# Optimization experiments

Hardware: AMD Instinct MI355X
Metric: run time of the kernel (lower is better)

Reference implementation:

```python
import jax, jax.numpy as jnp
import numpy as np

S = 4096      # total packed tokens
DIM = 1280    # hidden dim
H = 16        # num heads
HD = DIM // H # head dim = 80


def setup_inputs() -> dict:
    key = jax.random.key(0)
    ks = jax.random.split(key, 5)
    hidden_states = jax.random.normal(ks[0], (S, DIM), jnp.float32)
    # realistic rotary tables: [S, HD] with duplicated half-frequencies
    inv_freq = 1.0 / (10000.0 ** (np.arange(0, HD // 2, dtype=np.float64) / (HD // 2)))
    ang = np.arange(S, dtype=np.float64)[:, None] * inv_freq[None, :]          # [S, HD/2]
    emb = np.concatenate([ang, ang], axis=-1)                                   # [S, HD]
    cos = jnp.asarray(np.cos(emb), jnp.float32)
    sin = jnp.asarray(np.sin(emb), jnp.float32)
    scale = 1.0 / np.sqrt(DIM)
    qkv_w = jax.random.normal(ks[1], (3 * DIM, DIM), jnp.float32) * scale
    qkv_b = jax.random.normal(ks[2], (3 * DIM,), jnp.float32) * 0.02
    proj_w = jax.random.normal(ks[3], (DIM, DIM), jnp.float32) * scale
    proj_b = jax.random.normal(ks[4], (DIM,), jnp.float32) * 0.02
    # ragged segment boundaries: must start at 0 and end at S
    cu_seqlens = jnp.asarray([0, 300, 900, 1500, 2300, 2900, 3500, 4000, 4096], jnp.int32)
    return {
        "hidden_states": hidden_states,
        "cos": cos,
        "sin": sin,
        "qkv_w": qkv_w,
        "qkv_b": qkv_b,
        "proj_w": proj_w,
        "proj_b": proj_b,
        "cu_seqlens": cu_seqlens,
    }


def _rotate_half(x):
    x1, x2 = jnp.split(x, 2, axis=-1)
    return jnp.concatenate([-x2, x1], axis=-1)


def reference(hidden_states, cos, sin, qkv_w, qkv_b, proj_w, proj_b, cu_seqlens):
    seq_len, dim = hidden_states.shape
    hd = dim // H
    qkv = (hidden_states @ qkv_w.T + qkv_b).reshape(seq_len, 3, H, hd)
    q, k, v = qkv[:, 0], qkv[:, 1], qkv[:, 2]                 # each [S, H, hd]
    # RoPE in float32, broadcast cos/sin over heads
    c = cos[:, None, :].astype(jnp.float32)
    s = sin[:, None, :].astype(jnp.float32)
    qf = q.astype(jnp.float32)
    kf = k.astype(jnp.float32)
    q = (qf * c + _rotate_half(qf) * s).astype(q.dtype)
    k = (kf * c + _rotate_half(kf) * s).astype(k.dtype)
    # block-diagonal additive mask: segment id per token
    pos = jnp.arange(seq_len)
    seg = jnp.searchsorted(cu_seqlens[1:], pos, side='right')  # [S]
    neg = jnp.finfo(jnp.float32).min
    bias = jnp.where(seg[:, None] == seg[None, :], 0.0, neg)   # [S, S]
    attn = jnp.einsum('shd,thd->hst', q, k) / np.sqrt(hd) + bias[None]
    w = jax.nn.softmax(attn.astype(jnp.float32), axis=-1).astype(q.dtype)
    out = jnp.einsum('hst,thd->shd', w, v).reshape(seq_len, dim)
    return out @ proj_w.T + proj_b
```

## Files before the change

kernel.cpp:

```cpp
#include <hip/hip_runtime.h>
#include <hip/hip_bf16.h>
#include <stdint.h>

#define SQ 4096
#define DM 1280
#define NH 16
#define HDIM 80
#define N_QKV 3840

typedef __attribute__((ext_vector_type(8))) short short8;
typedef __attribute__((ext_vector_type(4))) float f32x4;

__device__ __forceinline__ unsigned short f2bf(float f) {
  union { float f; unsigned int u; } v; v.f = f;
  unsigned int r = v.u + 0x7FFFu + ((v.u >> 16) & 1u);
  return (unsigned short)(r >> 16);
}
__device__ __forceinline__ float bf2f(unsigned short u) {
  union { unsigned int u; float f; } v; v.u = ((unsigned int)u) << 16;
  return v.f;
}

__global__ __launch_bounds__(256) void cvt_all(const float* __restrict__ hidden,
                                               const float* __restrict__ qkv_w,
                                               const float* __restrict__ proj_w,
                                               unsigned short* __restrict__ oh,
                                               unsigned short* __restrict__ oq,
                                               unsigned short* __restrict__ op) {
  int b = blockIdx.x;
  const float* in;
  unsigned short* out;
  int base;
  if (b < 5120) { in = hidden; out = oh; base = b; }
  else if (b < 9920) { in = qkv_w; out = oq; base = b - 5120; }
  else { in = proj_w; out = op; base = b - 9920; }
  int i = base * 256 + threadIdx.x;
  float4 v = reinterpret_cast<const float4*>(in)[i];
  ushort4 o;
  o.x = f2bf(v.x); o.y = f2bf(v.y); o.z = f2bf(v.z); o.w = f2bf(v.w);
  reinterpret_cast<ushort4*>(out)[i] = o;
}

__device__ __forceinline__ void gload_lds16(const void* g, void* l) {
  __builtin_amdgcn_global_load_lds(
      (const __attribute__((address_space(1))) void*)g,
      (__attribute__((address_space(3))) void*)l, 16, 0, 0);
}

template <int OUT_BF16>
__global__ __launch_bounds__(256, 3) void gemm_bt(const unsigned short* __restrict__ A,
                                                  const unsigned short* __restrict__ B,
                                                  const float* __restrict__ bias,
                                                  void* __restrict__ C, int M, int N, int K,
                                                  int nbx) {
  __shared__ __align__(16) unsigned short As[3][128 * 32];
  __shared__ __align__(16) unsigned short Bs[3][128 * 32];
  const int tid = threadIdx.x;
  const int wave = tid >> 6, lane = tid & 63;
  const int r15 = lane & 15, kg = lane >> 4;
  const int wr = wave >> 1, wc = wave & 1;

  const int b = blockIdx.x;
  const int c = b & 7, i = b >> 3;
  const int by = (c & 3) * 8 + (i & 7);
  const int bx = (c >> 2) * (nbx >> 1) + (i >> 3);
  const int tm = by * 128, tn = bx * 128;

  f32x4 acc[4][4];
#pragma unroll
  for (int x = 0; x < 4; ++x)
#pragma unroll
    for (int j = 0; j < 4; ++j) acc[x][j] = {0.f, 0.f, 0.f, 0.f};

  const int slot0 = wave * 64 + lane;
  const int row0 = slot0 >> 2, k80 = (slot0 & 3) << 3;
  const int slot1 = slot0 + 256;
  const int row1 = slot1 >> 2, k81 = (slot1 & 3) << 3;
  const unsigned short* Arow0 = A + (size_t)(tm + row0) * K + k80;
  const unsigned short* Arow1 = A + (size_t)(tm + row1) * K + k81;
  const unsigned short* Brow0 = B + (size_t)(tn + row0) * K + k80;
  const unsigned short* Brow1 = B + (size_t)(tn + row1) * K + k81;
  const int ldsoff0 = (wave * 64) * 8;
  const int ldsoff1 = (wave * 64 + 256) * 8;

  auto stage = [&](int kt, int buf) {
    gload_lds16(Arow0 + kt, &As[buf][ldsoff0]);
    gload_lds16(Arow1 + kt, &As[buf][ldsoff1]);
    gload_lds16(Brow0 + kt, &Bs[buf][ldsoff0]);
    gload_lds16(Brow1 + kt, &Bs[buf][ldsoff1]);
  };

  const int nk = K >> 5;
  stage(0, 0);
  if (nk > 1) stage(32, 1);

  int buf = 0;
  for (int t = 0; t < nk; ++t) {
    if (t + 2 < nk) {
      stage((t + 2) << 5, (buf + 2) % 3);
      asm volatile("s_waitcnt vmcnt(8)" ::: "memory");
    } else if (t + 1 < nk) {
      asm volatile("s_waitcnt vmcnt(4)" ::: "memory");
    } else {
      asm volatile("s_waitcnt vmcnt(0)" ::: "memory");
    }
    __builtin_amdgcn_sched_barrier(0);
    __builtin_amdgcn_s_barrier();

    short8 af[4], bfr[4];
#pragma unroll
    for (int mi = 0; mi < 4; ++mi)
      af[mi] = *reinterpret_cast<const short8*>(&As[buf][(wr * 64 + mi * 16 + r15) * 32 + kg * 8]);
#pragma unroll
    for (int ni = 0; ni < 4; ++ni)
      bfr[ni] = *reinterpret_cast<const short8*>(&Bs[buf][(wc * 64 + ni * 16 + r15) * 32 + kg * 8]);
    __builtin_amdgcn_s_setprio(1);
#pragma unroll
    for (int mi = 0; mi < 4; ++mi)
#pragma unroll
      for (int ni = 0; ni < 4; ++ni)
        acc[mi][ni] = __builtin_amdgcn_mfma_f32_16x16x32_bf16(af[mi], bfr[ni], acc[mi][ni], 0, 0, 0);
    __builtin_amdgcn_s_setprio(0);

    __builtin_amdgcn_s_barrier();
    __builtin_amdgcn_sched_barrier(0);
    buf = (buf + 1) % 3;
  }

#pragma unroll
  for (int mi = 0; mi < 4; ++mi) {
#pragma unroll
    for (int ni = 0; ni < 4; ++ni) {
      int col = tn + wc * 64 + ni * 16 + r15;
      float bv = bias[col];
#pragma unroll
      for (int r = 0; r < 4; ++r) {
        int row = tm + wr * 64 + mi * 16 + kg * 4 + r;
        float v = acc[mi][ni][r] + bv;
        if (OUT_BF16)
          ((unsigned short*)C)[(size_t)row * N + col] = f2bf(v);
        else
          ((float*)C)[(size_t)row * N + col] = v;
      }
    }
  }
}

__global__ __launch_bounds__(256) void rope_v_kernel(unsigned short* __restrict__ qkv,
                                                     const float* __restrict__ cosb,
                                                     const float* __restrict__ sinb,
                                                     unsigned short* __restrict__ Vt) {
  int h = blockIdx.y, s0 = blockIdx.x * 64;
  __shared__ unsigned short vt[64][80];
  for (int e = threadIdx.x; e < 64 * 40; e += 256) {
    int sl = e / 40, dp = e % 40;
    int s = s0 + sl;
    float c = cosb[s * HDIM + dp];
    float sn = sinb[s * HDIM + dp];
    size_t qb = (size_t)s * N_QKV + h * HDIM;
    float q1 = bf2f(qkv[qb + dp]), q2 = bf2f(qkv[qb + dp + 40]);
    qkv[qb + dp] = f2bf(q1 * c - q2 * sn);
    qkv[qb + dp + 40] = f2bf(q2 * c + q1 * sn);
    size_t kb = qb + DM;
    float k1 = bf2f(qkv[kb + dp]), k2 = bf2f(qkv[kb + dp + 40]);
    qkv[kb + dp] = f2bf(k1 * c - k2 * sn);
    qkv[kb + dp + 40] = f2bf(k2 * c + k1 * sn);
    size_t vb = qb + 2 * DM;
    vt[sl][dp] = qkv[vb + dp];
    vt[sl][dp + 40] = qkv[vb + dp + 40];
  }
  __syncthreads();
  for (int e = threadIdx.x; e < HDIM * 64; e += 256) {
    int d = e >> 6, sl = e & 63;
    Vt[((size_t)h * HDIM + d) * SQ + s0 + sl] = vt[sl][d];
  }
}

template <int CTRL>
__device__ __forceinline__ float dpp_f(float x) {
  int xi = __builtin_bit_cast(int, x);
  int r = __builtin_amdgcn_update_dpp(xi, xi, CTRL, 0xf, 0xf, true);
  return __builtin_bit_cast(float, r);
}
__device__ __forceinline__ float rowmax16(float x) {
  x = fmaxf(x, dpp_f<0xB1>(x));
  x = fmaxf(x, dpp_f<0x4E>(x));
  x = fmaxf(x, dpp_f<0x141>(x));
  x = fmaxf(x, dpp_f<0x140>(x));
  return x;
}
__device__ __forceinline__ float rowsum16(float x) {
  x += dpp_f<0xB1>(x);
  x += dpp_f<0x4E>(x);
  x += dpp_f<0x141>(x);
  x += dpp_f<0x140>(x);
  return x;
}

__global__ __launch_bounds__(256, 2) void attn_kernel(const unsigned short* __restrict__ qkv,
                                                      const unsigned short* __restrict__ Vt,
                                                      const int* __restrict__ cu, int nseg,
                                                      unsigned short* __restrict__ attn_out) {
  constexpr int PROW = 68;
  __shared__ __align__(16) unsigned char Kl[2][64 * 256];
  __shared__ __align__(16) unsigned char Vl[2][80 * 128];
  __shared__ __align__(16) unsigned short Pl[4][16 * PROW];
  __shared__ int cus[32];

  const int tid = threadIdx.x;
  const int wave = tid >> 6, lane = tid & 63;
  const int r15 = lane & 15, kg = lane >> 4;
  const int s7 = r15 & 7;
  const short8 z8 = {0, 0, 0, 0, 0, 0, 0, 0};

  const int b = blockIdx.x;
  const int xcd = b & 7, j = b >> 3;
  const int h = xcd * 2 + (j >> 6);
  const int qt = j & 63;

  if (tid <= nseg) cus[tid] = cu[tid];
  __syncthreads();

  auto seg_of = [&](int pos) {
    int s2 = 0;
    for (int i2 = 1; i2 < nseg; ++i2)
      if (pos >= cus[i2]) s2 = i2;
    return s2;
  };

  const int tbase = qt * 64;
  const int wbase = tbase + wave * 16;
  int rs[4], re[4];
#pragma unroll
  for (int r = 0; r < 4; ++r) {
    int sg = seg_of(wbase + kg * 4 + r);
    rs[r] = cus[sg];
    re[r] = cus[sg + 1];
  }
  const int kb0 = cus[seg_of(tbase)] & ~63;
  const int kend = cus[seg_of(tbase + 63) + 1];
  const int nt = (kend - kb0 + 63) >> 6;

  const unsigned short* qp = qkv + (size_t)(wbase + r15) * N_QKV + h * HDIM;
  short8 qf[3];
#pragma unroll
  for (int ds = 0; ds < 3; ++ds) {
    int d0 = ds * 32 + kg * 8;
    qf[ds] = (d0 < HDIM) ? *reinterpret_cast<const short8*>(qp + d0) : z8;
  }

  float m[4] = {-1e30f, -1e30f, -1e30f, -1e30f};
  float l[4] = {0.f, 0.f, 0.f, 0.f};
  f32x4 acc[5];
#pragma unroll
  for (int dg = 0; dg < 5; ++dg) acc[dg] = {0.f, 0.f, 0.f, 0.f};

  const float scale = 0.1118033988749895f;
  const unsigned short* kbase = qkv + DM + (size_t)h * HDIM;
  const unsigned short* vbase = Vt + (size_t)h * HDIM * SQ;
  unsigned short* pw = &Pl[wave][0];
  const int wub = tid & ~63;

  auto issue_stage = [&](int kb, int buf) {
    unsigned char* kd = &Kl[buf][0];
    unsigned char* vd = &Vl[buf][0];
#pragma unroll
    for (int p = 0; p < 4; ++p) {
      int L = p * 256 + tid;
      int row = L >> 4;
      int c = (L & 15) ^ (row & 7);
      int csrc = (c < 10) ? c : 0;
      gload_lds16(kbase + (size_t)(kb + row) * N_QKV + csrc * 8,
                  kd + (p * 256 + wub) * 16);
    }
#pragma unroll
    for (int p = 0; p < 2; ++p) {
      int L = p * 256 + tid;
      int row = L >> 3;
      int c = (L & 7) ^ (row & 7);
      gload_lds16(vbase + (size_t)row * SQ + kb + c * 8,
                  vd + (p * 256 + wub) * 16);
    }
    {
      int L = 512 + (wub >> 1) + (lane & 31);
      int row = L >> 3;
      int c = (L & 7) ^ (row & 7);
      if (lane < 32)
        gload_lds16(vbase + (size_t)row * SQ + kb + c * 8,
                    vd + (512 + (wub >> 1)) * 16);
    }
  };

  issue_stage(kb0, 0);
  int cur = 0;

  for (int t = 0; t < nt; ++t) {
    const int k0 = kb0 + (t << 6);
    if (t + 1 < nt) {
      issue_stage(k0 + 64, cur ^ 1);
      asm volatile("s_waitcnt vmcnt(7)" ::: "memory");
    } else {
      asm volatile("s_waitcnt vmcnt(0)" ::: "memory");
    }
    __builtin_amdgcn_sched_barrier(0);
    __builtin_amdgcn_s_barrier();

    const unsigned char* Kc = &Kl[cur][0];
    const unsigned char* Vc = &Vl[cur][0];

    f32x4 sa[4];
#pragma unroll
    for (int g = 0; g < 4; ++g) sa[g] = {0.f, 0.f, 0.f, 0.f};
#pragma unroll
    for (int g = 0; g < 4; ++g) {
      const unsigned char* kr = Kc + ((g * 16 + r15) << 8);
#pragma unroll
      for (int ds = 0; ds < 3; ++ds) {
        int d0 = ds * 32 + kg * 8;
        short8 kf = (d0 < HDIM)
            ? *reinterpret_cast<const short8*>(kr + (((ds * 4 + kg) ^ s7) << 4))
            : z8;
        sa[g] = __builtin_amdgcn_mfma_f32_16x16x32_bf16(qf[ds], kf, sa[g], 0, 0, 0);
      }
    }

    short8 vf[5][2];
#pragma unroll
    for (int dg = 0; dg < 5; ++dg)
#pragma unroll
      for (int g2 = 0; g2 < 2; ++g2)
        vf[dg][g2] = *reinterpret_cast<const short8*>(
            Vc + ((dg * 16 + r15) << 7) + (((g2 * 4 + kg) ^ s7) << 4));

    float p[4][4], corr[4];
#pragma unroll
    for (int r = 0; r < 4; ++r) {
      float vv[4];
#pragma unroll
      for (int g = 0; g < 4; ++g) {
        int key = k0 + g * 16 + r15;
        vv[g] = (key >= rs[r] && key < re[r]) ? sa[g][r] * scale : -1e30f;
      }
      float mx = fmaxf(fmaxf(vv[0], vv[1]), fmaxf(vv[2], vv[3]));
      mx = rowmax16(mx);
      float mn = fmaxf(m[r], mx);
      float c = __expf(m[r] - mn);
      float sm = 0.f;
#pragma unroll
      for (int g = 0; g < 4; ++g) {
        p[r][g] = __expf(vv[g] - mn);
        sm += p[r][g];
      }
      sm = rowsum16(sm);
      l[r] = l[r] * c + sm;
      m[r] = mn;
      corr[r] = c;
    }
#pragma unroll
    for (int dg = 0; dg < 5; ++dg) {
      f32x4 t2 = acc[dg];
      t2[0] *= corr[0]; t2[1] *= corr[1]; t2[2] *= corr[2]; t2[3] *= corr[3];
      acc[dg] = t2;
    }

#pragma unroll
    for (int r = 0; r < 4; ++r) {
      unsigned short* prow = pw + (kg * 4 + r) * PROW;
#pragma unroll
      for (int g = 0; g < 4; ++g) prow[g * 16 + r15] = f2bf(p[r][g]);
    }
    asm volatile("s_waitcnt lgkmcnt(0)" ::: "memory");
    __builtin_amdgcn_sched_barrier(0);
    const unsigned short* prd = pw + r15 * PROW;
    union { short8 v; uint2 d[2]; } pu[2];
#pragma unroll
    for (int g2 = 0; g2 < 2; ++g2) {
      pu[g2].d[0] = *reinterpret_cast<const uint2*>(prd + g2 * 32 + kg * 8);
      pu[g2].d[1] = *reinterpret_cast<const uint2*>(prd + g2 * 32 + kg * 8 + 4);
    }

    __builtin_amdgcn_s_setprio(1);
#pragma unroll
    for (int dg = 0; dg < 5; ++dg)
#pragma unroll
      for (int g2 = 0; g2 < 2; ++g2)
        acc[dg] = __builtin_amdgcn_mfma_f32_16x16x32_bf16(pu[g2].v, vf[dg][g2], acc[dg], 0, 0, 0);
    __builtin_amdgcn_s_setprio(0);

    __builtin_amdgcn_s_barrier();
    cur ^= 1;
  }

#pragma unroll
  for (int r = 0; r < 4; ++r) {
    int row = wbase + kg * 4 + r;
    float inv = 1.0f / l[r];
#pragma unroll
    for (int dg = 0; dg < 5; ++dg)
      attn_out[(size_t)row * DM + h * HDIM + dg * 16 + r15] = f2bf(acc[dg][r] * inv);
  }
}

extern "C" void kernel_launch(void* const* d_in, const int* in_sizes, int n_in,
                              void* d_out, int out_size, void* d_ws, size_t ws_size,
                              hipStream_t stream) {
  const float* hidden = (const float*)d_in[0];
  const float* cosb = (const float*)d_in[1];
  const float* sinb = (const float*)d_in[2];
  const float* qkv_w = (const float*)d_in[3];
  const float* qkv_b = (const float*)d_in[4];
  const float* proj_w = (const float*)d_in[5];
  const float* proj_b = (const float*)d_in[6];
  const int* cu = (const int*)d_in[7];
  int nseg = in_sizes[7] - 1;
  float* out = (float*)d_out;

  char* ws = (char*)d_ws;
  unsigned short* Ah = (unsigned short*)(ws);
  unsigned short* Wq = (unsigned short*)(ws + 10485760);
  unsigned short* Wp = (unsigned short*)(ws + 10485760 + 9830400);
  unsigned short* qkvB = (unsigned short*)(ws + 23592960);
  unsigned short* Vt = (unsigned short*)(ws + 23592960 + 31457280);
  unsigned short* attn_out = Ah;

  cvt_all<<<dim3(11520), dim3(256), 0, stream>>>(hidden, qkv_w, proj_w, Ah, Wq, Wp);
  gemm_bt<1><<<dim3(960), dim3(256), 0, stream>>>(Ah, Wq, qkv_b, qkvB, SQ, N_QKV, DM, 30);
  rope_v_kernel<<<dim3(64, NH), dim3(256), 0, stream>>>(qkvB, cosb, sinb, Vt);
  attn_kernel<<<dim3(1024), dim3(256), 0, stream>>>(qkvB, Vt, cu, nseg, attn_out);
  gemm_bt<0><<<dim3(320), dim3(256), 0, stream>>>(attn_out, Wp, proj_b, out, SQ, DM, DM, 10);
}
```

Baseline: 193.7 us.

## Restructure attention loop: skip inactive tiles, defer rescale, load V directly to registers

Folds the softmax scale into Q during RoPE, removes the V shared-memory staging so V fragments are read from global memory straight into registers, and raises the occupancy target to 3 blocks per CU. Each wave now skips key tiles that fall outside its own segment range. Tiles fully inside a segment drop the masking, and when the new row max stays within a threshold of the running max, the accumulator rescale is skipped (lazy rescaling). The P buffer gets an XOR swizzle so it can be read with 16-byte loads. The risks are global-load latency for V, a shallower prefetch pipeline since the K stage is issued later and waited on with vmcnt(0), and register pressure under the tighter launch bound.

After: 306.1 us. +58.0%, slower.

```diff
diff --git a/kernel.cpp b/kernel.cpp
--- a/kernel.cpp
+++ b/kernel.cpp
@@ -150,6 +150,7 @@
                                                      const float* __restrict__ cosb,
                                                      const float* __restrict__ sinb,
                                                      unsigned short* __restrict__ Vt) {
+  const float SC = 0.1118033988749895f;
   int h = blockIdx.y, s0 = blockIdx.x * 64;
   __shared__ unsigned short vt[64][80];
   for (int e = threadIdx.x; e < 64 * 40; e += 256) {
@@ -159,8 +160,8 @@
     float sn = sinb[s * HDIM + dp];
     size_t qb = (size_t)s * N_QKV + h * HDIM;
     float q1 = bf2f(qkv[qb + dp]), q2 = bf2f(qkv[qb + dp + 40]);
-    qkv[qb + dp] = f2bf(q1 * c - q2 * sn);
-    qkv[qb + dp + 40] = f2bf(q2 * c + q1 * sn);
+    qkv[qb + dp] = f2bf((q1 * c - q2 * sn) * SC);
+    qkv[qb + dp + 40] = f2bf((q2 * c + q1 * sn) * SC);
     size_t kb = qb + DM;
     float k1 = bf2f(qkv[kb + dp]), k2 = bf2f(qkv[kb + dp + 40]);
     qkv[kb + dp] = f2bf(k1 * c - k2 * sn);
@@ -197,14 +198,12 @@
   return x;
 }
 
-__global__ __launch_bounds__(256, 2) void attn_kernel(const unsigned short* __restrict__ qkv,
+__global__ __launch_bounds__(256, 3) void attn_kernel(const unsigned short* __restrict__ qkv,
                                                       const unsigned short* __restrict__ Vt,
                                                       const int* __restrict__ cu, int nseg,
                                                       unsigned short* __restrict__ attn_out) {
-  constexpr int PROW = 68;
   __shared__ __align__(16) unsigned char Kl[2][64 * 256];
-  __shared__ __align__(16) unsigned char Vl[2][80 * 128];
-  __shared__ __align__(16) unsigned short Pl[4][16 * PROW];
+  __shared__ __align__(16) unsigned short Pl[4][16 * 64];
   __shared__ int cus[32];
 
   const int tid = threadIdx.x;
@@ -237,6 +236,10 @@
     rs[r] = cus[sg];
     re[r] = cus[sg + 1];
   }
+  const int seg_lo = seg_of(wbase), seg_hi = seg_of(wbase + 15);
+  const int w_lo = cus[seg_lo], w_hi = cus[seg_hi + 1];
+  const int rs_hi = cus[seg_hi], re_lo = cus[seg_lo + 1];
+
   const int kb0 = cus[seg_of(tbase)] & ~63;
   const int kend = cus[seg_of(tbase + 63) + 1];
   const int nt = (kend - kb0 + 63) >> 6;
@@ -255,7 +258,6 @@
 #pragma unroll
   for (int dg = 0; dg < 5; ++dg) acc[dg] = {0.f, 0.f, 0.f, 0.f};
 
-  const float scale = 0.1118033988749895f;
   const unsigned short* kbase = qkv + DM + (size_t)h * HDIM;
   const unsigned short* vbase = Vt + (size_t)h * HDIM * SQ;
   unsigned short* pw = &Pl[wave][0];
@@ -263,7 +265,6 @@
 
   auto issue_stage = [&](int kb, int buf) {
     unsigned char* kd = &Kl[buf][0];
-    unsigned char* vd = &Vl[buf][0];
 #pragma unroll
     for (int p = 0; p < 4; ++p) {
       int L = p * 256 + tid;
@@ -273,22 +274,6 @@
       gload_lds16(kbase + (size_t)(kb + row) * N_QKV + csrc * 8,
                   kd + (p * 256 + wub) * 16);
     }
-#pragma unroll
-    for (int p = 0; p < 2; ++p) {
-      int L = p * 256 + tid;
-      int row = L >> 3;
-      int c = (L & 7) ^ (row & 7);
-      gload_lds16(vbase + (size_t)row * SQ + kb + c * 8,
-                  vd + (p * 256 + wub) * 16);
-    }
-    {
-      int L = 512 + (wub >> 1) + (lane & 31);
-      int row = L >> 3;
-      int c = (L & 7) ^ (row & 7);
-      if (lane < 32)
-        gload_lds16(vbase + (size_t)row * SQ + kb + c * 8,
-                    vd + (512 + (wub >> 1)) * 16);
-    }
   };
 
   issue_stage(kb0, 0);
@@ -296,96 +281,130 @@
 
   for (int t = 0; t < nt; ++t) {
     const int k0 = kb0 + (t << 6);
-    if (t + 1 < nt) {
-      issue_stage(k0 + 64, cur ^ 1);
-      asm volatile("s_waitcnt vmcnt(7)" ::: "memory");
-    } else {
-      asm volatile("s_waitcnt vmcnt(0)" ::: "memory");
-    }
+    asm volatile("s_waitcnt vmcnt(0)" ::: "memory");
     __builtin_amdgcn_sched_barrier(0);
     __builtin_amdgcn_s_barrier();
 
-    const unsigned char* Kc = &Kl[cur][0];
-    const unsigned char* Vc = &Vl[cur][0];
-
-    f32x4 sa[4];
-#pragma unroll
-    for (int g = 0; g < 4; ++g) sa[g] = {0.f, 0.f, 0.f, 0.f};
-#pragma unroll
-    for (int g = 0; g < 4; ++g) {
-      const unsigned char* kr = Kc + ((g * 16 + r15) << 8);
-#pragma unroll
-      for (int ds = 0; ds < 3; ++ds) {
-        int d0 = ds * 32 + kg * 8;
-        short8 kf = (d0 < HDIM)
-            ? *reinterpret_cast<const short8*>(kr + (((ds * 4 + kg) ^ s7) << 4))
-            : z8;
-        sa[g] = __builtin_amdgcn_mfma_f32_16x16x32_bf16(qf[ds], kf, sa[g], 0, 0, 0);
+    const bool active = (k0 < w_hi) && (k0 + 64 > w_lo);
+
+    if (active) {
+      short8 vf[5][2];
+#pragma unroll
+      for (int dg = 0; dg < 5; ++dg)
+#pragma unroll
+        for (int g2 = 0; g2 < 2; ++g2)
+          vf[dg][g2] = *reinterpret_cast<const short8*>(
+              vbase + (size_t)(dg * 16 + r15) * SQ + k0 + g2 * 32 + kg * 8);
+
+      if (t + 1 < nt) issue_stage(k0 + 64, cur ^ 1);
+
+      const unsigned char* Kc = &Kl[cur][0];
+      f32x4 sa[4];
+#pragma unroll
+      for (int g = 0; g < 4; ++g) sa[g] = {0.f, 0.f, 0.f, 0.f};
+      __builtin_amdgcn_s_setprio(1);
+#pragma unroll
+      for (int g = 0; g < 4; ++g) {
+        const unsigned char* kr = Kc + ((g * 16 + r15) << 8);
+#pragma unroll
+        for (int ds = 0; ds < 3; ++ds) {
+          int d0 = ds * 32 + kg * 8;
+          short8 kf = (d0 < HDIM)
+              ? *reinterpret_cast<const short8*>(kr + (((ds * 4 + kg) ^ s7) << 4))
+              : z8;
+          sa[g] = __builtin_amdgcn_mfma_f32_16x16x32_bf16(qf[ds], kf, sa[g], 0, 0, 0);
+        }
       }
+      __builtin_amdgcn_s_setprio(0);
+
+      const bool interior = (k0 >= rs_hi) && (k0 + 64 <= re_lo);
+      float p[4][4], corr[4];
+      bool resc;
+      if (interior) {
+        float mx4[4];
+#pragma unroll
+        for (int r = 0; r < 4; ++r)
+          mx4[r] = rowmax16(fmaxf(fmaxf(sa[0][r], sa[1][r]), fmaxf(sa[2][r], sa[3][r])));
+        int defer = (mx4[0] <= m[0] + 8.f) && (mx4[1] <= m[1] + 8.f) &&
+                    (mx4[2] <= m[2] + 8.f) && (mx4[3] <= m[3] + 8.f);
+        if (__all(defer)) {
+          resc = false;
+#pragma unroll
+          for (int r = 0; r < 4; ++r) {
+            float sm = 0.f;
+#pragma unroll
+            for (int g = 0; g < 4; ++g) { p[r][g] = __expf(sa[g][r] - m[r]); sm += p[r][g]; }
+            l[r] += rowsum16(sm);
+          }
+        } else {
+          resc = true;
+#pragma unroll
+          for (int r = 0; r < 4; ++r) {
+            float mn = fmaxf(m[r], mx4[r]);
+            corr[r] = __expf(m[r] - mn);
+            float sm = 0.f;
+#pragma unroll
+            for (int g = 0; g < 4; ++g) { p[r][g] = __expf(sa[g][r] - mn); sm += p[r][g]; }
+            l[r] = l[r] * corr[r] + rowsum16(sm);
+            m[r] = mn;
+          }
+        }
+      } else {
+        resc = true;
+#pragma unroll
+        for (int r = 0; r < 4; ++r) {
+          float vv[4];
+#pragma unroll
+          for (int g = 0; g < 4; ++g) {
+            int key = k0 + g * 16 + r15;
+            vv[g] = (key >= rs[r] && key < re[r]) ? sa[g][r] : -1e30f;
+          }
+          float mx = rowmax16(fmaxf(fmaxf(vv[0], vv[1]), fmaxf(vv[2], vv[3])));
+          float mn = fmaxf(m[r], mx);
+          corr[r] = __expf(m[r] - mn);
+          float sm = 0.f;
+#pragma unroll
+          for (int g = 0; g < 4; ++g) { p[r][g] = __expf(vv[g] - mn); sm += p[r][g]; }
+          l[r] = l[r] * corr[r] + rowsum16(sm);
+          m[r] = mn;
+        }
+      }
+      if (resc) {
+#pragma unroll
+        for (int dg = 0; dg < 5; ++dg) {
+          f32x4 t2 = acc[dg];
+          t2[0] *= corr[0]; t2[1] *= corr[1]; t2[2] *= corr[2]; t2[3] *= corr[3];
+          acc[dg] = t2;
+        }
+      }
+
+#pragma unroll
+      for (int r = 0; r < 4; ++r) {
+        int row = kg * 4 + r;
+        unsigned short* prow = pw + row * 64;
+        int rsw = row & 7;
+#pragma unroll
+        for (int g = 0; g < 4; ++g)
+          prow[(((g * 2 + (r15 >> 3)) ^ rsw) << 3) + (r15 & 7)] = f2bf(p[r][g]);
+      }
+      asm volatile("s_waitcnt lgkmcnt(0)" ::: "memory");
+      __builtin_amdgcn_sched_barrier(0);
+      short8 pu[2];
+#pragma unroll
+      for (int g2 = 0; g2 < 2; ++g2)
+        pu[g2] = *reinterpret_cast<const short8*>(
+            pw + r15 * 64 + (((g2 * 4 + kg) ^ s7) << 3));
+
+      __builtin_amdgcn_s_setprio(1);
+#pragma unroll
+      for (int dg = 0; dg < 5; ++dg)
+#pragma unroll
+        for (int g2 = 0; g2 < 2; ++g2)
+          acc[dg] = __builtin_amdgcn_mfma_f32_16x16x32_bf16(pu[g2], vf[dg][g2], acc[dg], 0, 0, 0);
+      __builtin_amdgcn_s_setprio(0);
+    } else {
+      if (t + 1 < nt) issue_stage(k0 + 64, cur ^ 1);
     }
-
-    short8 vf[5][2];
-#pragma unroll
-    for (int dg = 0; dg < 5; ++dg)
-#pragma unroll
-      for (int g2 = 0; g2 < 2; ++g2)
-        vf[dg][g2] = *reinterpret_cast<const short8*>(
-            Vc + ((dg * 16 + r15) << 7) + (((g2 * 4 + kg) ^ s7) << 4));
-
-    float p[4][4], corr[4];
-#pragma unroll
-    for (int r = 0; r < 4; ++r) {
-      float vv[4];
-#pragma unroll
-      for (int g = 0; g < 4; ++g) {
-        int key = k0 + g * 16 + r15;
-        vv[g] = (key >= rs[r] && key < re[r]) ? sa[g][r] * scale : -1e30f;
-      }
-      float mx = fmaxf(fmaxf(vv[0], vv[1]), fmaxf(vv[2], vv[3]));
-      mx = rowmax16(mx);
-      float mn = fmaxf(m[r], mx);
-      float c = __expf(m[r] - mn);
-      float sm = 0.f;
-#pragma unroll
-      for (int g = 0; g < 4; ++g) {
-        p[r][g] = __expf(vv[g] - mn);
-        sm += p[r][g];
-      }
-      sm = rowsum16(sm);
-      l[r] = l[r] * c + sm;
-      m[r] = mn;
-      corr[r] = c;
-    }
-#pragma unroll
-    for (int dg = 0; dg < 5; ++dg) {
-      f32x4 t2 = acc[dg];
-      t2[0] *= corr[0]; t2[1] *= corr[1]; t2[2] *= corr[2]; t2[3] *= corr[3];
-      acc[dg] = t2;
-    }
-
-#pragma unroll
-    for (int r = 0; r < 4; ++r) {
-      unsigned short* prow = pw + (kg * 4 + r) * PROW;
-#pragma unroll
-      for (int g = 0; g < 4; ++g) prow[g * 16 + r15] = f2bf(p[r][g]);
-    }
-    asm volatile("s_waitcnt lgkmcnt(0)" ::: "memory");
-    __builtin_amdgcn_sched_barrier(0);
-    const unsigned short* prd = pw + r15 * PROW;
-    union { short8 v; uint2 d[2]; } pu[2];
-#pragma unroll
-    for (int g2 = 0; g2 < 2; ++g2) {
-      pu[g2].d[0] = *reinterpret_cast<const uint2*>(prd + g2 * 32 + kg * 8);
-      pu[g2].d[1] = *reinterpret_cast<const uint2*>(prd + g2 * 32 + kg * 8 + 4);
-    }
-
-    __builtin_amdgcn_s_setprio(1);
-#pragma unroll
-    for (int dg = 0; dg < 5; ++dg)
-#pragma unroll
-      for (int g2 = 0; g2 < 2; ++g2)
-        acc[dg] = __builtin_amdgcn_mfma_f32_16x16x32_bf16(pu[g2].v, vf[dg][g2], acc[dg], 0, 0, 0);
-    __builtin_amdgcn_s_setprio(0);
 
     __builtin_amdgcn_s_barrier();
     cur ^= 1;
```
